# Kernel tuning notes

Measured on AMD Instinct MI355X. Metric: run time of the kernel, lower is better.

## Reference

```python
import jax, jax.numpy as jnp
import numpy as np

ALPHA = 0.25
GAMMA = 2.0
EPS_CLIP = 1e-4


def calc_iou(a, b):
    # a: [A,4] anchors, b: [M,4] gt boxes, boxes are [x1,y1,x2,y2]
    area = (b[:, 2] - b[:, 0]) * (b[:, 3] - b[:, 1])  # [M]
    iw = jnp.minimum(a[:, None, 2], b[None, :, 2]) - jnp.maximum(a[:, None, 0], b[None, :, 0])
    ih = jnp.minimum(a[:, None, 3], b[None, :, 3]) - jnp.maximum(a[:, None, 1], b[None, :, 1])
    iw = jnp.maximum(iw, 0.0)
    ih = jnp.maximum(ih, 0.0)
    ua = ((a[:, 2] - a[:, 0]) * (a[:, 3] - a[:, 1]))[:, None] + area[None, :] - iw * ih
    ua = jnp.maximum(ua, 1e-8)
    return iw * ih / ua  # [A,M]


def _per_image(cls_p, reg_p, ann, anchor):
    # cls_p [A,C], reg_p [A,4], ann [M,5], anchor [A,4]
    aw = anchor[:, 2] - anchor[:, 0]
    ah = anchor[:, 3] - anchor[:, 1]
    acx = anchor[:, 0] + 0.5 * aw
    acy = anchor[:, 1] + 0.5 * ah

    valid = ann[:, 4] != -1.0            # [M] padding mask
    has_ann = jnp.any(valid)

    cls_p = jnp.clip(cls_p, EPS_CLIP, 1.0 - EPS_CLIP)

    iou = calc_iou(anchor, ann[:, :4])   # [A,M]
    iou = jnp.where(valid[None, :], iou, -1.0)  # invalid gt never matched
    iou_max = jnp.max(iou, axis=1)       # [A]
    iou_arg = jnp.argmax(iou, axis=1)    # [A]
    assigned = ann[iou_arg]              # [A,5]

    neg = iou_max < 0.4
    pos = iou_max >= 0.5
    num_pos = jnp.sum(pos.astype(jnp.float32))

    C = cls_p.shape[1]
    targets = jnp.full_like(cls_p, -1.0)
    targets = jnp.where(neg[:, None], 0.0, targets)
    targets = jnp.where(pos[:, None], 0.0, targets)
    cls_idx = assigned[:, 4].astype(jnp.int32)
    onehot = (jnp.arange(C)[None, :] == cls_idx[:, None]) & pos[:, None]
    targets = jnp.where(onehot, 1.0, targets)

    alpha_f = jnp.where(targets == 1.0, ALPHA, 1.0 - ALPHA)
    focal_w = alpha_f * jnp.where(targets == 1.0, 1.0 - cls_p, cls_p) ** GAMMA
    bce = -(targets * jnp.log(cls_p) + (1.0 - targets) * jnp.log(1.0 - cls_p))
    cls_loss = jnp.where(targets != -1.0, focal_w * bce, 0.0)
    cls_l = jnp.where(has_ann, jnp.sum(cls_loss) / jnp.maximum(num_pos, 1.0), 0.0)

    gw0 = assigned[:, 2] - assigned[:, 0]
    gh0 = assigned[:, 3] - assigned[:, 1]
    gcx = assigned[:, 0] + 0.5 * gw0
    gcy = assigned[:, 1] + 0.5 * gh0
    gw = jnp.maximum(gw0, 1.0)
    gh = jnp.maximum(gh0, 1.0)
    tdx = (gcx - acx) / aw
    tdy = (gcy - acy) / ah
    tdw = jnp.log(gw / aw)
    tdh = jnp.log(gh / ah)
    norm = jnp.array([0.1, 0.1, 0.2, 0.2], dtype=cls_p.dtype)
    rt = jnp.stack([tdx, tdy, tdw, tdh], axis=1) / norm  # [A,4]

    diff = jnp.abs(rt - reg_p)
    sl1 = jnp.where(diff <= 1.0 / 9.0, 0.5 * 9.0 * diff * diff, diff - 0.5 / 9.0)
    reg_sum = jnp.sum(sl1 * pos[:, None].astype(sl1.dtype))
    reg_l = jnp.where(has_ann & (num_pos > 0), reg_sum / jnp.maximum(num_pos * 4.0, 1.0), 0.0)
    return cls_l, reg_l


def setup_inputs() -> dict:
    key = jax.random.key(0)
    ks = jax.random.split(key, 10)
    B, A, C, M = 8, 49104, 90, 32
    IMG = 512.0

    classifications = jax.random.uniform(ks[0], (B, A, C), dtype=jnp.float32)
    regressions = jax.random.normal(ks[1], (B, A, 4), dtype=jnp.float32)

    # anchors: valid boxes [x1,y1,x2,y2]
    acx = jax.random.uniform(ks[2], (A,), minval=0.0, maxval=IMG)
    acy = jax.random.uniform(ks[3], (A,), minval=0.0, maxval=IMG)
    asz = jax.random.uniform(ks[4], (A, 2), minval=16.0, maxval=128.0)
    anchors = jnp.stack([acx - 0.5 * asz[:, 0], acy - 0.5 * asz[:, 1],
                         acx + 0.5 * asz[:, 0], acy + 0.5 * asz[:, 1]], axis=1)[None].astype(jnp.float32)

    # annotations: [x1,y1,x2,y2,label], label=-1 marks padding
    gx1 = jax.random.uniform(ks[5], (B, M), minval=0.0, maxval=IMG - 64.0)
    gy1 = jax.random.uniform(ks[6], (B, M), minval=0.0, maxval=IMG - 64.0)
    gwh = jax.random.uniform(ks[7], (B, M, 2), minval=16.0, maxval=64.0)
    labels = jax.random.randint(ks[8], (B, M), 0, C).astype(jnp.float32)
    invalid = jax.random.uniform(ks[9], (B, M)) < 0.25
    labels = jnp.where(invalid, -1.0, labels)
    labels = labels.at[:, 0].set(jnp.abs(labels[:, 0]))  # ensure >=1 valid gt per image
    annotations = jnp.concatenate([gx1[..., None], gy1[..., None],
                                   (gx1 + gwh[..., 0])[..., None],
                                   (gy1 + gwh[..., 1])[..., None],
                                   labels[..., None]], axis=-1).astype(jnp.float32)

    return {"classifications": classifications, "regressions": regressions,
            "anchors": anchors, "annotations": annotations}


def reference(classifications, regressions, anchors, annotations):
    cls_l, reg_l = jax.vmap(_per_image, in_axes=(0, 0, 0, None))(
        classifications, regressions, annotations, anchors[0])
    return (jnp.mean(cls_l, keepdims=True), jnp.mean(reg_l, keepdims=True))
```

## Files before the change

### kernel.cpp

```cpp
#include <hip/hip_runtime.h>

constexpr int B = 8;
constexpr int A = 49104;
constexpr int C = 90;
constexpr int M = 32;
constexpr float EPS_CLIP = 1e-4f;
constexpr float LN2 = 0.6931471805599453f;

constexpr int TPB = 256;
constexpr int N4_TOT = B * A * C / 4;
constexpr int N4_IMG = A * C / 4;
constexpr int SL4 = 4096;
constexpr int NSTREAM = (N4_TOT + SL4 - 1) / SL4;
constexpr int APT = 4;
constexpr int AB_ANCH = TPB * APT;
constexpr int ABPI = (A + AB_ANCH - 1) / AB_ANCH;
constexpr int NANCH = ABPI * B;

typedef float f32x4 __attribute__((ext_vector_type(4)));


__device__ __forceinline__ float clampp(float v) {
    return fminf(fmaxf(v, EPS_CLIP), 1.f - EPS_CLIP);
}

__device__ __forceinline__ float neg4(f32x4 v) {
    float s = 0.f;
#pragma unroll
    for (int j = 0; j < 4; ++j) {
        const float p = clampp(v[j]);
        s = fmaf(p * p, __log2f(1.f - p), s);
    }
    return s;
}

__global__ __launch_bounds__(TPB) void focal_main_kernel(
    const float* __restrict__ cls,
    const float* __restrict__ reg,
    const float* __restrict__ anc,
    const float* __restrict__ ann,
    float* __restrict__ accum)
{
    __shared__ float s_ann[M * 5];
    __shared__ float s_red[3][TPB / 64];
    __shared__ int   s_list[AB_ANCH];
    __shared__ int   s_cnt;

    const int t    = threadIdx.x;
    const int wid  = t >> 6;
    const int lane = t & 63;
    const int blk  = blockIdx.x;

    if (blk < NANCH) {
        const int b     = blk / ABPI;
        const int abase = (blk - b * ABPI) * AB_ANCH;

        if (t < M * 5) s_ann[t] = ann[b * M * 5 + t];
        if (t == 0) s_cnt = 0;
        __syncthreads();

        float corr = 0.f, reg_sum = 0.f, pos_cnt = 0.f;

        float4 ab4[APT];
        float  awk[APT], ahk[APT], areaA[APT], best[APT];
        int    argm[APT];
        bool   act[APT];
#pragma unroll
        for (int k = 0; k < APT; ++k) {
            const int a = abase + t + k * TPB;
            act[k] = (a < A);
            ab4[k] = act[k] ? reinterpret_cast<const float4*>(anc)[a]
                            : make_float4(0.f, 0.f, 0.f, 0.f);
            awk[k] = ab4[k].z - ab4[k].x;
            ahk[k] = ab4[k].w - ab4[k].y;
            areaA[k] = awk[k] * ahk[k];
            best[k] = -INFINITY;
            argm[k] = 0;
        }

        for (int m = 0; m < M; ++m) {
            const float bx1 = s_ann[m * 5 + 0];
            const float by1 = s_ann[m * 5 + 1];
            const float bx2 = s_ann[m * 5 + 2];
            const float by2 = s_ann[m * 5 + 3];
            const float lab = s_ann[m * 5 + 4];
            const float areaB = (bx2 - bx1) * (by2 - by1);
            const bool  vgt = (lab != -1.0f);
#pragma unroll
            for (int k = 0; k < APT; ++k) {
                float iw = fminf(ab4[k].z, bx2) - fmaxf(ab4[k].x, bx1);
                float ih = fminf(ab4[k].w, by2) - fmaxf(ab4[k].y, by1);
                iw = fmaxf(iw, 0.f);
                ih = fmaxf(ih, 0.f);
                const float inter = iw * ih;
                const float ua = fmaxf(areaA[k] + areaB - inter, 1e-8f);
                const float iou = inter / ua;
                const float val = vgt ? iou : -1.0f;
                if (val > best[k]) { best[k] = val; argm[k] = m; }
            }
        }

#pragma unroll
        for (int k = 0; k < APT; ++k) {
            if (!act[k]) continue;
            const int a = abase + t + k * TPB;
            if (best[k] >= 0.5f) {
                pos_cnt += 1.f;
                const int am = argm[k];
                const float gx1 = s_ann[am * 5 + 0];
                const float gy1 = s_ann[am * 5 + 1];
                const float gx2 = s_ann[am * 5 + 2];
                const float gy2 = s_ann[am * 5 + 3];
                const float acx = ab4[k].x + 0.5f * awk[k];
                const float acy = ab4[k].y + 0.5f * ahk[k];
                const float gw0 = gx2 - gx1;
                const float gh0 = gy2 - gy1;
                const float gcx = gx1 + 0.5f * gw0;
                const float gcy = gy1 + 0.5f * gh0;
                const float gw = fmaxf(gw0, 1.f);
                const float gh = fmaxf(gh0, 1.f);
                const float4 rp = reinterpret_cast<const float4*>(reg)[(size_t)b * A + a];
                const float rt0 = (gcx - acx) / awk[k] * 10.f;
                const float rt1 = (gcy - acy) / ahk[k] * 10.f;
                const float rt2 = __logf(gw / awk[k]) * 5.f;
                const float rt3 = __logf(gh / ahk[k]) * 5.f;
                const float d0 = fabsf(rt0 - rp.x);
                const float d1 = fabsf(rt1 - rp.y);
                const float d2 = fabsf(rt2 - rp.z);
                const float d3 = fabsf(rt3 - rp.w);
                auto sl1 = [](float d) {
                    return (d <= (1.f / 9.f)) ? 4.5f * d * d : d - (0.5f / 9.f);
                };
                reg_sum += sl1(d0) + sl1(d1) + sl1(d2) + sl1(d3);

                const int cidx = (int)s_ann[am * 5 + 4];
                const float p = clampp(cls[((size_t)b * A + a) * C + cidx]);
                corr += 0.75f * LN2 * (p * p * __log2f(1.f - p))
                      + 0.25f * (1.f - p) * (1.f - p) * (-__logf(p));
            } else if (best[k] >= 0.4f) {
                const int slot = atomicAdd(&s_cnt, 1);
                s_list[slot] = t + k * TPB;
            }
        }
        __syncthreads();

        const int cnt = s_cnt;
        for (int i = wid; i < cnt; i += TPB / 64) {
            const int aidx = s_list[i];
            const float* row = cls + ((size_t)b * A + abase + aidx) * (size_t)C;
            float s = 0.f;
            if (lane < C) {
                const float p = clampp(row[lane]);
                s = p * p * __log2f(1.f - p);
            }
            if (lane + 64 < C) {
                const float p = clampp(row[lane + 64]);
                s = fmaf(p * p, __log2f(1.f - p), s);
            }
            for (int off = 32; off; off >>= 1) s += __shfl_down(s, off);
            if (lane == 0) corr += 0.75f * LN2 * s;
        }

        float v0 = corr, v1 = reg_sum, v2 = pos_cnt;
        for (int off = 32; off; off >>= 1) {
            v0 += __shfl_down(v0, off);
            v1 += __shfl_down(v1, off);
            v2 += __shfl_down(v2, off);
        }
        if (lane == 0) { s_red[0][wid] = v0; s_red[1][wid] = v1; s_red[2][wid] = v2; }
        __syncthreads();
        if (t == 0) {
            float a0 = 0.f, a1 = 0.f, a2 = 0.f;
            for (int w = 0; w < TPB / 64; ++w) {
                a0 += s_red[0][w]; a1 += s_red[1][w]; a2 += s_red[2][w];
            }
            atomicAdd(&accum[B + b],     a0);
            atomicAdd(&accum[2 * B + b], a1);
            atomicAdd(&accum[3 * B + b], a2);
        }
        return;
    }

    const int sblk = blk - NANCH;
    const f32x4* __restrict__ cls4 = reinterpret_cast<const f32x4*>(cls);
    const int sbase = sblk * SL4;
    const int nsl   = min(SL4, N4_TOT - sbase);
    const int img0  = sbase / N4_IMG;
    const int imgL  = (sbase + nsl - 1) / N4_IMG;

    float acc0 = 0.f, acc1 = 0.f;
    if (img0 == imgL) {
        const f32x4* p = cls4 + sbase + t;
        int i = t;
        float accA = 0.f, accB = 0.f;
        for (; i + 7 * TPB < nsl; i += 8 * TPB) {
            f32x4 v[8];
#pragma unroll
            for (int k = 0; k < 8; ++k) v[k] = p[k * TPB];
            p += 8 * TPB;
#pragma unroll
            for (int k = 0; k < 8; ++k) {
                if (k & 1) accB += neg4(v[k]); else accA += neg4(v[k]);
            }
        }
        for (; i < nsl; i += TPB) { accA += neg4(*p); p += TPB; }
        acc0 = accA + accB;
    } else {
        const int split = (img0 + 1) * N4_IMG;
        for (int i = t; i < nsl; i += TPB) {
            const float s = neg4(cls4[sbase + i]);
            if (sbase + i < split) acc0 += s; else acc1 += s;
        }
    }

    float w0 = acc0, w1 = acc1;
    for (int off = 32; off; off >>= 1) {
        w0 += __shfl_down(w0, off);
        w1 += __shfl_down(w1, off);
    }
    if (lane == 0) { s_red[0][wid] = w0; s_red[1][wid] = w1; }
    __syncthreads();
    if (t == 0) {
        float a0 = 0.f, a1 = 0.f;
        for (int w = 0; w < TPB / 64; ++w) { a0 += s_red[0][w]; a1 += s_red[1][w]; }
        atomicAdd(&accum[img0], a0);
        if (imgL != img0) atomicAdd(&accum[imgL], a1);
    }
}

__global__ void focal_finalize_kernel(const float* __restrict__ ann,
                                      const float* __restrict__ accum,
                                      float* __restrict__ out)
{
    const int t = threadIdx.x;
    float cls_l = 0.f, reg_l = 0.f;
    if (t < B) {
        bool has = false;
        for (int m = 0; m < M; ++m)
            has = has || (ann[t * M * 5 + m * 5 + 4] != -1.0f);
        const float S    = accum[t];
        const float corr = accum[B + t];
        const float rs   = accum[2 * B + t];
        const float np   = accum[3 * B + t];
        const float cls_sum = -0.75f * LN2 * S + corr;
        cls_l = has ? cls_sum / fmaxf(np, 1.f) : 0.f;
        reg_l = (has && np > 0.f) ? rs / fmaxf(np * 4.f, 1.f) : 0.f;
    }
    for (int off = 4; off; off >>= 1) {
        cls_l += __shfl_down(cls_l, off);
        reg_l += __shfl_down(reg_l, off);
    }
    if (t == 0) {
        out[0] = cls_l * (1.f / B);
        out[1] = reg_l * (1.f / B);
    }
}

extern "C" void kernel_launch(void* const* d_in, const int* in_sizes, int n_in,
                              void* d_out, int out_size, void* d_ws, size_t ws_size,
                              hipStream_t stream) {
    const float* cls = (const float*)d_in[0];
    const float* reg = (const float*)d_in[1];
    const float* anc = (const float*)d_in[2];
    const float* ann = (const float*)d_in[3];
    float* out = (float*)d_out;
    float* accum = (float*)d_ws;

    (void)hipMemsetAsync(accum, 0, 4 * B * sizeof(float), stream);

    focal_main_kernel<<<dim3(NANCH + NSTREAM), TPB, 0, stream>>>(cls, reg, anc, ann, accum);
    focal_finalize_kernel<<<1, 64, 0, stream>>>(ann, accum, out);
}
```

Before: 54.51 us.

## Fuse finalize into main kernel via last-block counter and reorder block roles

Drops the separate finalize kernel launch. The main kernel now ends with a threadfence and an atomic completion counter, and the last block to finish computes the final losses. Block ordering also changes so streaming blocks come first and anchor-matching blocks come last, which alters scheduling and tail behavior. This saves one launch and its inter-kernel gap, but adds a global atomic and fence in every block.

```diff
diff --git a/kernel.cpp b/kernel.cpp
--- a/kernel.cpp
+++ b/kernel.cpp
@@ -16,6 +16,7 @@
 constexpr int AB_ANCH = TPB * APT;
 constexpr int ABPI = (A + AB_ANCH - 1) / AB_ANCH;
 constexpr int NANCH = ABPI * B;
+constexpr int NTOTB = NSTREAM + NANCH;
 
 typedef float f32x4 __attribute__((ext_vector_type(4)));
 
@@ -39,21 +40,69 @@
     const float* __restrict__ reg,
     const float* __restrict__ anc,
     const float* __restrict__ ann,
-    float* __restrict__ accum)
+    float* __restrict__ accum,
+    float* __restrict__ out)
 {
     __shared__ float s_ann[M * 5];
     __shared__ float s_red[3][TPB / 64];
     __shared__ int   s_list[AB_ANCH];
     __shared__ int   s_cnt;
+    __shared__ int   s_last;
 
     const int t    = threadIdx.x;
     const int wid  = t >> 6;
     const int lane = t & 63;
     const int blk  = blockIdx.x;
 
-    if (blk < NANCH) {
-        const int b     = blk / ABPI;
-        const int abase = (blk - b * ABPI) * AB_ANCH;
+    if (blk < NSTREAM) {
+        const f32x4* __restrict__ cls4 = reinterpret_cast<const f32x4*>(cls);
+        const int sbase = blk * SL4;
+        const int nsl   = min(SL4, N4_TOT - sbase);
+        const int img0  = sbase / N4_IMG;
+        const int imgL  = (sbase + nsl - 1) / N4_IMG;
+
+        float acc0 = 0.f, acc1 = 0.f;
+        if (img0 == imgL) {
+            const f32x4* p = cls4 + sbase + t;
+            int i = t;
+            float accA = 0.f, accB = 0.f;
+            for (; i + 7 * TPB < nsl; i += 8 * TPB) {
+                f32x4 v[8];
+#pragma unroll
+                for (int k = 0; k < 8; ++k) v[k] = p[k * TPB];
+                p += 8 * TPB;
+#pragma unroll
+                for (int k = 0; k < 8; ++k) {
+                    if (k & 1) accB += neg4(v[k]); else accA += neg4(v[k]);
+                }
+            }
+            for (; i < nsl; i += TPB) { accA += neg4(*p); p += TPB; }
+            acc0 = accA + accB;
+        } else {
+            const int split = (img0 + 1) * N4_IMG;
+            for (int i = t; i < nsl; i += TPB) {
+                const float s = neg4(cls4[sbase + i]);
+                if (sbase + i < split) acc0 += s; else acc1 += s;
+            }
+        }
+
+        float w0 = acc0, w1 = acc1;
+        for (int off = 32; off; off >>= 1) {
+            w0 += __shfl_down(w0, off);
+            w1 += __shfl_down(w1, off);
+        }
+        if (lane == 0) { s_red[0][wid] = w0; s_red[1][wid] = w1; }
+        __syncthreads();
+        if (t == 0) {
+            float a0 = 0.f, a1 = 0.f;
+            for (int w = 0; w < TPB / 64; ++w) { a0 += s_red[0][w]; a1 += s_red[1][w]; }
+            atomicAdd(&accum[img0], a0);
+            if (imgL != img0) atomicAdd(&accum[imgL], a1);
+        }
+    } else {
+        const int ablk  = blk - NSTREAM;
+        const int b     = ablk / ABPI;
+        const int abase = (ablk - b * ABPI) * AB_ANCH;
 
         if (t < M * 5) s_ann[t] = ann[b * M * 5 + t];
         if (t == 0) s_cnt = 0;
@@ -178,81 +227,39 @@
             atomicAdd(&accum[2 * B + b], a1);
             atomicAdd(&accum[3 * B + b], a2);
         }
-        return;
-    }
-
-    const int sblk = blk - NANCH;
-    const f32x4* __restrict__ cls4 = reinterpret_cast<const f32x4*>(cls);
-    const int sbase = sblk * SL4;
-    const int nsl   = min(SL4, N4_TOT - sbase);
-    const int img0  = sbase / N4_IMG;
-    const int imgL  = (sbase + nsl - 1) / N4_IMG;
-
-    float acc0 = 0.f, acc1 = 0.f;
-    if (img0 == imgL) {
-        const f32x4* p = cls4 + sbase + t;
-        int i = t;
-        float accA = 0.f, accB = 0.f;
-        for (; i + 7 * TPB < nsl; i += 8 * TPB) {
-            f32x4 v[8];
-#pragma unroll
-            for (int k = 0; k < 8; ++k) v[k] = p[k * TPB];
-            p += 8 * TPB;
-#pragma unroll
-            for (int k = 0; k < 8; ++k) {
-                if (k & 1) accB += neg4(v[k]); else accA += neg4(v[k]);
-            }
-        }
-        for (; i < nsl; i += TPB) { accA += neg4(*p); p += TPB; }
-        acc0 = accA + accB;
-    } else {
-        const int split = (img0 + 1) * N4_IMG;
-        for (int i = t; i < nsl; i += TPB) {
-            const float s = neg4(cls4[sbase + i]);
-            if (sbase + i < split) acc0 += s; else acc1 += s;
-        }
-    }
-
-    float w0 = acc0, w1 = acc1;
-    for (int off = 32; off; off >>= 1) {
-        w0 += __shfl_down(w0, off);
-        w1 += __shfl_down(w1, off);
-    }
-    if (lane == 0) { s_red[0][wid] = w0; s_red[1][wid] = w1; }
+    }
+
+    if (t == 0) {
+        __threadfence();
+        int* ctr = reinterpret_cast<int*>(accum + 36);
+        const int done = atomicAdd(ctr, 1);
+        s_last = (done == NTOTB - 1) ? 1 : 0;
+    }
     __syncthreads();
-    if (t == 0) {
-        float a0 = 0.f, a1 = 0.f;
-        for (int w = 0; w < TPB / 64; ++w) { a0 += s_red[0][w]; a1 += s_red[1][w]; }
-        atomicAdd(&accum[img0], a0);
-        if (imgL != img0) atomicAdd(&accum[imgL], a1);
-    }
-}
-
-__global__ void focal_finalize_kernel(const float* __restrict__ ann,
-                                      const float* __restrict__ accum,
-                                      float* __restrict__ out)
-{
-    const int t = threadIdx.x;
-    float cls_l = 0.f, reg_l = 0.f;
-    if (t < B) {
-        bool has = false;
-        for (int m = 0; m < M; ++m)
-            has = has || (ann[t * M * 5 + m * 5 + 4] != -1.0f);
-        const float S    = accum[t];
-        const float corr = accum[B + t];
-        const float rs   = accum[2 * B + t];
-        const float np   = accum[3 * B + t];
-        const float cls_sum = -0.75f * LN2 * S + corr;
-        cls_l = has ? cls_sum / fmaxf(np, 1.f) : 0.f;
-        reg_l = (has && np > 0.f) ? rs / fmaxf(np * 4.f, 1.f) : 0.f;
-    }
-    for (int off = 4; off; off >>= 1) {
-        cls_l += __shfl_down(cls_l, off);
-        reg_l += __shfl_down(reg_l, off);
-    }
-    if (t == 0) {
-        out[0] = cls_l * (1.f / B);
-        out[1] = reg_l * (1.f / B);
+    if (s_last) {
+        float cls_l = 0.f, reg_l = 0.f;
+        if (t < B) {
+            bool has = false;
+            for (int m = 0; m < M; ++m)
+                has = has || (ann[t * M * 5 + m * 5 + 4] != -1.0f);
+            const float S    = atomicAdd(&accum[t],         0.f);
+            const float corr = atomicAdd(&accum[B + t],     0.f);
+            const float rs   = atomicAdd(&accum[2 * B + t], 0.f);
+            const float np   = atomicAdd(&accum[3 * B + t], 0.f);
+            const float cls_sum = -0.75f * LN2 * S + corr;
+            cls_l = has ? cls_sum / fmaxf(np, 1.f) : 0.f;
+            reg_l = (has && np > 0.f) ? rs / fmaxf(np * 4.f, 1.f) : 0.f;
+        }
+        if (t < 64) {
+            for (int off = 4; off; off >>= 1) {
+                cls_l += __shfl_down(cls_l, off);
+                reg_l += __shfl_down(reg_l, off);
+            }
+            if (t == 0) {
+                out[0] = cls_l * (1.f / B);
+                out[1] = reg_l * (1.f / B);
+            }
+        }
     }
 }
 
@@ -266,8 +273,7 @@
     float* out = (float*)d_out;
     float* accum = (float*)d_ws;
 
-    (void)hipMemsetAsync(accum, 0, 4 * B * sizeof(float), stream);
-
-    focal_main_kernel<<<dim3(NANCH + NSTREAM), TPB, 0, stream>>>(cls, reg, anc, ann, accum);
-    focal_finalize_kernel<<<1, 64, 0, stream>>>(ann, accum, out);
-}
+    (void)hipMemsetAsync(accum, 0, 40 * sizeof(float), stream);
+
+    focal_main_kernel<<<dim3(NTOTB), TPB, 0, stream>>>(cls, reg, anc, ann, accum, out);
+}
```

Result: slower. 115.1 us (+111.2%).
